# Optimization experiments

Hardware: AMD Instinct MI355X
Metric: run time of the kernel (lower is better)

The kernel has to match this reference:

```python
import jax, jax.numpy as jnp
import numpy as np

B, S, D, H = 2, 2048, 1024, 16
DK = D // H

def setup_inputs() -> dict:
    key = jax.random.key(0)
    ks = jax.random.split(key, 5)
    scale = 1.0 / np.sqrt(D)
    return {
        "query": jax.random.normal(ks[0], (B, S, D), dtype=jnp.float32),
        "mask": jnp.ones((B, S, S), dtype=jnp.int32),
        "Wq": jax.random.normal(ks[1], (D, D), dtype=jnp.float32) * scale,
        "bq": jnp.zeros((D,), dtype=jnp.float32),
        "Wk": jax.random.normal(ks[2], (D, D), dtype=jnp.float32) * scale,
        "bk": jnp.zeros((D,), dtype=jnp.float32),
        "Wv": jax.random.normal(ks[3], (D, D), dtype=jnp.float32) * scale,
        "bv": jnp.zeros((D,), dtype=jnp.float32),
        "Wo": jax.random.normal(ks[4], (D, D), dtype=jnp.float32) * scale,
        "bo": jnp.zeros((D,), dtype=jnp.float32),
    }

def reference(query, mask, Wq, bq, Wk, bk, Wv, bv, Wo, bo):
    # self-attention: key = value = query (torch Linear: x @ W.T + b)
    b, s, d = query.shape
    def proj(x, W, bias):
        y = jnp.einsum('bsd,ed->bse', x, W) + bias
        return y.reshape(b, s, H, DK).transpose(0, 2, 1, 3)  # [B,H,S,DK]
    q = proj(query, Wq, bq)
    k = proj(query, Wk, bk)
    v = proj(query, Wv, bv)
    scores = jnp.einsum('bhqd,bhkd->bhqk', q, k) / jnp.sqrt(jnp.float32(DK))
    m = mask[:, None, :, :]  # [B,1,S,S] (torch unsqueeze(1) for 3D mask)
    scores = jnp.where(m == 0, jnp.float32(-1e9), scores)
    w = jax.nn.softmax(scores, axis=-1)  # dropout: eval mode -> identity
    o = jnp.einsum('bhqk,bhkd->bhqd', w, v)
    o = o.transpose(0, 2, 1, 3).reshape(b, s, d)
    return jnp.einsum('bsd,ed->bse', o, Wo) + bo
```

## Files before the change

### kernel.cpp

```cpp
#include <hip/hip_runtime.h>


typedef _Float16 f16x8 __attribute__((ext_vector_type(8)));
typedef _Float16 f16x4 __attribute__((ext_vector_type(4)));
typedef float    f32x4 __attribute__((ext_vector_type(4)));

#define MFMA16(a, b, c) __builtin_amdgcn_mfma_f32_16x16x32_f16(a, b, c, 0, 0, 0)

__device__ __forceinline__ void gld16(const void* g, void* l) {
    __builtin_amdgcn_global_load_lds(
        (const __attribute__((address_space(1))) void*)g,
        (__attribute__((address_space(3))) void*)l, 16, 0, 0);
}

__global__ void k_conv(const float* __restrict__ in, _Float16* __restrict__ out, int n) {
    int i = (blockIdx.x * 256 + threadIdx.x) * 4;
    if (i >= n) return;
    float4 v = *(const float4*)(in + i);
    f16x4 o;
    o.x = (_Float16)v.x; o.y = (_Float16)v.y; o.z = (_Float16)v.z; o.w = (_Float16)v.w;
    *(f16x4*)(out + i) = o;
}

__global__ void k_maskscan(const int* __restrict__ mask, int* __restrict__ flag) {
    int i = (blockIdx.x * 256 + threadIdx.x) * 4;
    int4 v = *(const int4*)(mask + i);
    if ((v.x == 0) | (v.y == 0) | (v.z == 0) | (v.w == 0)) atomicOr(flag, 1);
}

__global__ __launch_bounds__(256, 2) void k_qkv(
    const _Float16* __restrict__ X,
    const _Float16* __restrict__ Wqh, const _Float16* __restrict__ Wkh,
    const _Float16* __restrict__ Wvh,
    const float* __restrict__ bq, const float* __restrict__ bk,
    const float* __restrict__ bv,
    _Float16* __restrict__ Qo, _Float16* __restrict__ Ko, _Float16* __restrict__ Vo)
{
    __shared__ _Float16 As[128 * 64];
    __shared__ _Float16 Bs[128 * 64];
    const int tid = threadIdx.x;
    const int lane = tid & 63, wv = tid >> 6;
    const int wrow = wv >> 1, wcol = wv & 1;
    const int quad = lane >> 4, lc = lane & 15;
    const int which = blockIdx.x >> 3;
    const _Float16* W   = which == 0 ? Wqh : which == 1 ? Wkh : Wvh;
    const float*   bias = which == 0 ? bq  : which == 1 ? bk  : bv;
    const int n0 = (blockIdx.x & 7) * 128;
    const int m0 = blockIdx.y * 128;

    const f32x4 fzero = {0.f, 0.f, 0.f, 0.f};
    f32x4 acc[4][4];
#pragma unroll
    for (int a = 0; a < 4; ++a)
#pragma unroll
        for (int bb = 0; bb < 4; ++bb) acc[a][bb] = fzero;

#pragma unroll 1
    for (int k0 = 0; k0 < 1024; k0 += 64) {
        __syncthreads();
#pragma unroll
        for (int it = 0; it < 4; ++it) {
            const int wbase = it * 256 + wv * 64;
            const int ci = wbase + lane;
            const int r = ci >> 3;
            const int c8 = (((ci & 7) ^ (r & 7)) * 8);
            gld16(X + (size_t)(m0 + r) * 1024 + k0 + c8, As + wbase * 8);
            gld16(W + (size_t)(n0 + r) * 1024 + k0 + c8, Bs + wbase * 8);
        }
        __syncthreads();
#pragma unroll
        for (int ks = 0; ks < 2; ++ks) {
            f16x8 af[4], bf[4];
#pragma unroll
            for (int mt = 0; mt < 4; ++mt)
                af[mt] = *(const f16x8*)(As + (wrow * 64 + mt * 16 + lc) * 64 +
                                         (((ks * 4 + quad) ^ (lc & 7)) * 8));
#pragma unroll
            for (int nt = 0; nt < 4; ++nt)
                bf[nt] = *(const f16x8*)(Bs + (wcol * 64 + nt * 16 + lc) * 64 +
                                         (((ks * 4 + quad) ^ (lc & 7)) * 8));
#pragma unroll
            for (int mt = 0; mt < 4; ++mt)
#pragma unroll
                for (int nt = 0; nt < 4; ++nt)
                    acc[mt][nt] = MFMA16(af[mt], bf[nt], acc[mt][nt]);
        }
    }
    const float qs = (which == 0) ? 0.18033688011112042f : 1.0f;
    if (which == 2) {
#pragma unroll
        for (int nt = 0; nt < 4; ++nt) {
            const int e = n0 + wcol * 64 + nt * 16 + lc;
            const float bv_ = bias[e];
            const int h = e >> 6, dk = e & 63;
#pragma unroll
            for (int mt = 0; mt < 4; ++mt)
#pragma unroll
                for (int i = 0; i < 4; ++i) {
                    const int m = m0 + wrow * 64 + mt * 16 + quad * 4 + i;
                    const int b_ = m >> 11, s = m & 2047;
                    Vo[(((size_t)b_ * 16 + h) * 64 + dk) * 2048 + s] =
                        (_Float16)(acc[mt][nt][i] + bv_);
                }
        }
    } else {
        _Float16* Out = which == 0 ? Qo : Ko;
#pragma unroll
        for (int nt = 0; nt < 4; ++nt) {
            const int e = n0 + wcol * 64 + nt * 16 + lc;
            const float bv_ = bias[e];
            const int h = e >> 6, dk = e & 63;
#pragma unroll
            for (int mt = 0; mt < 4; ++mt)
#pragma unroll
                for (int i = 0; i < 4; ++i) {
                    const int m = m0 + wrow * 64 + mt * 16 + quad * 4 + i;
                    const int b_ = m >> 11, s = m & 2047;
                    Out[(((size_t)b_ * 16 + h) * 2048 + s) * 64 + dk] =
                        (_Float16)((acc[mt][nt][i] + bv_) * qs);
                }
        }
    }
}

__global__ __launch_bounds__(256, 2) void k_oproj(
    const _Float16* __restrict__ Oin, const _Float16* __restrict__ Woh,
    const float* __restrict__ bo, float* __restrict__ out)
{
    __shared__ _Float16 As[128 * 64];
    __shared__ _Float16 Bs[128 * 64];
    const int tid = threadIdx.x;
    const int lane = tid & 63, wv = tid >> 6;
    const int wrow = wv >> 1, wcol = wv & 1;
    const int quad = lane >> 4, lc = lane & 15;
    const int n0 = blockIdx.x * 128;
    const int m0 = blockIdx.y * 128;

    const f32x4 fzero = {0.f, 0.f, 0.f, 0.f};
    f32x4 acc[4][4];
#pragma unroll
    for (int a = 0; a < 4; ++a)
#pragma unroll
        for (int bb = 0; bb < 4; ++bb) acc[a][bb] = fzero;

#pragma unroll 1
    for (int k0 = 0; k0 < 1024; k0 += 64) {
        __syncthreads();
#pragma unroll
        for (int it = 0; it < 4; ++it) {
            const int wbase = it * 256 + wv * 64;
            const int ci = wbase + lane;
            const int r = ci >> 3;
            const int c8 = (((ci & 7) ^ (r & 7)) * 8);
            gld16(Oin + (size_t)(m0 + r) * 1024 + k0 + c8, As + wbase * 8);
            gld16(Woh + (size_t)(n0 + r) * 1024 + k0 + c8, Bs + wbase * 8);
        }
        __syncthreads();
#pragma unroll
        for (int ks = 0; ks < 2; ++ks) {
            f16x8 af[4], bf[4];
#pragma unroll
            for (int mt = 0; mt < 4; ++mt)
                af[mt] = *(const f16x8*)(As + (wrow * 64 + mt * 16 + lc) * 64 +
                                         (((ks * 4 + quad) ^ (lc & 7)) * 8));
#pragma unroll
            for (int nt = 0; nt < 4; ++nt)
                bf[nt] = *(const f16x8*)(Bs + (wcol * 64 + nt * 16 + lc) * 64 +
                                         (((ks * 4 + quad) ^ (lc & 7)) * 8));
#pragma unroll
            for (int mt = 0; mt < 4; ++mt)
#pragma unroll
                for (int nt = 0; nt < 4; ++nt)
                    acc[mt][nt] = MFMA16(af[mt], bf[nt], acc[mt][nt]);
        }
    }
#pragma unroll
    for (int nt = 0; nt < 4; ++nt) {
        const int e = n0 + wcol * 64 + nt * 16 + lc;
        const float bv_ = bo[e];
#pragma unroll
        for (int mt = 0; mt < 4; ++mt)
#pragma unroll
            for (int i = 0; i < 4; ++i) {
                const int m = m0 + wrow * 64 + mt * 16 + quad * 4 + i;
                out[(size_t)m * 1024 + e] = acc[mt][nt][i] + bv_;
            }
    }
}

__global__ __launch_bounds__(256, 3) void k_attn(
    const _Float16* __restrict__ Q, const _Float16* __restrict__ K,
    const _Float16* __restrict__ Vt, const int* __restrict__ mask,
    const int* __restrict__ flag, _Float16* __restrict__ O)
{
    __shared__ _Float16 Ks[128 * 64];
    __shared__ _Float16 Vs[64 * 128];
    __shared__ _Float16 Ps[4][32 * 64];

    const int tid = threadIdx.x;
    const int lane = tid & 63, wv = tid >> 6;
    const int quad = lane >> 4, lc = lane & 15;
    const int bh = blockIdx.y;
    const int b = bh >> 4, h = bh & 15;
    const int q0 = blockIdx.x * 128;

    const _Float16* Qb = Q  + (size_t)bh * 2048 * 64;
    const _Float16* Kb = K  + (size_t)bh * 2048 * 64;
    const _Float16* Vb = Vt + (size_t)bh * 64 * 2048;

    f16x8 qf[2][2];
#pragma unroll
    for (int nb = 0; nb < 2; ++nb)
#pragma unroll
        for (int ks = 0; ks < 2; ++ks)
            qf[nb][ks] = *(const f16x8*)(Qb + (size_t)(q0 + wv * 32 + nb * 16 + lc) * 64 +
                                         ks * 32 + quad * 8);

    const f32x4 fzero = {0.f, 0.f, 0.f, 0.f};
    f32x4 o[2][4];
    float m_i[2], l_i[2];
#pragma unroll
    for (int nb = 0; nb < 2; ++nb) { m_i[nb] = -1e30f; l_i[nb] = 0.f; }
#pragma unroll
    for (int qb = 0; qb < 2; ++qb)
#pragma unroll
        for (int db = 0; db < 4; ++db) o[qb][db] = fzero;

    const bool has_zero = (*flag != 0);
    _Float16* Pw = Ps[wv];

#pragma unroll 1
    for (int kt = 0; kt < 16; ++kt) {
        const int k0 = kt * 128;
        __syncthreads();
#pragma unroll
        for (int it = 0; it < 4; ++it) {
            const int p = it * 256 + wv * 64 + lane;
            const int r = p >> 3, c = (p & 7) ^ (r & 7);
            gld16(Kb + (size_t)(k0 + r) * 64 + c * 8, Ks + (it * 256 + wv * 64) * 8);
        }
#pragma unroll
        for (int it = 0; it < 4; ++it) {
            const int p = it * 256 + wv * 64 + lane;
            const int dk = p >> 4, c = (p & 15) ^ (dk & 15);
            gld16(Vb + (size_t)dk * 2048 + k0 + c * 8, Vs + (it * 256 + wv * 64) * 8);
        }
        __syncthreads();

        f32x4 st[8][2];
#pragma unroll
        for (int mb = 0; mb < 8; ++mb)
#pragma unroll
            for (int nb = 0; nb < 2; ++nb) st[mb][nb] = fzero;
#pragma unroll
        for (int ks = 0; ks < 2; ++ks)
#pragma unroll
            for (int mb = 0; mb < 8; ++mb) {
                f16x8 kf = *(const f16x8*)(Ks + (mb * 16 + lc) * 64 +
                                           (((ks * 4 + quad) ^ (lc & 7)) * 8));
                st[mb][0] = MFMA16(kf, qf[0][ks], st[mb][0]);
                st[mb][1] = MFMA16(kf, qf[1][ks], st[mb][1]);
            }

        if (has_zero) {
            for (int nb = 0; nb < 2; ++nb) {
                const int q = q0 + wv * 32 + nb * 16 + lc;
                const int* mr = mask + ((size_t)b * 2048 + q) * 2048 + k0;
                for (int mb = 0; mb < 8; ++mb)
                    for (int i = 0; i < 4; ++i)
                        if (mr[mb * 16 + quad * 4 + i] == 0) st[mb][nb][i] = -1e30f;
            }
        }

        float alpha[2];
#pragma unroll
        for (int nb = 0; nb < 2; ++nb) {
            float v = st[0][nb][0];
#pragma unroll
            for (int mb = 0; mb < 8; ++mb)
#pragma unroll
                for (int i = 0; i < 4; ++i) v = fmaxf(v, st[mb][nb][i]);
            v = fmaxf(v, __shfl_xor(v, 16));
            v = fmaxf(v, __shfl_xor(v, 32));
            const float mnew = fmaxf(m_i[nb], v);
            alpha[nb] = exp2f(m_i[nb] - mnew);
            m_i[nb] = mnew;
            float rs = 0.f;
#pragma unroll
            for (int mb = 0; mb < 8; ++mb)
#pragma unroll
                for (int i = 0; i < 4; ++i) {
                    const float p = exp2f(st[mb][nb][i] - mnew);
                    st[mb][nb][i] = p;
                    rs += p;
                }
            rs += __shfl_xor(rs, 16);
            rs += __shfl_xor(rs, 32);
            l_i[nb] = l_i[nb] * alpha[nb] + rs;
        }
#pragma unroll
        for (int qb = 0; qb < 2; ++qb)
#pragma unroll
            for (int i = 0; i < 4; ++i) {
                const float aC = __shfl(alpha[qb], quad * 4 + i);
#pragma unroll
                for (int db = 0; db < 4; ++db) o[qb][db][i] *= aC;
            }

#pragma unroll
        for (int ph = 0; ph < 2; ++ph) {
#pragma unroll
            for (int nb = 0; nb < 2; ++nb) {
                const int r = nb * 16 + lc;
#pragma unroll
                for (int mbl = 0; mbl < 4; ++mbl) {
                    const int mb = ph * 4 + mbl;
                    const int cp = (2 * mbl + (quad >> 1)) ^ (lc & 7);
                    f16x4 pk;
#pragma unroll
                    for (int i = 0; i < 4; ++i) pk[i] = (_Float16)st[mb][nb][i];
                    *(f16x4*)(Pw + r * 64 + cp * 8 + (quad & 1) * 4) = pk;
                }
            }
#pragma unroll
            for (int kcl = 0; kcl < 2; ++kcl) {
                const int kc = ph * 2 + kcl;
                f16x8 pa[2];
#pragma unroll
                for (int qb = 0; qb < 2; ++qb)
                    pa[qb] = *(const f16x8*)(Pw + (qb * 16 + lc) * 64 +
                                             (((kcl * 4 + quad) ^ (lc & 7)) * 8));
#pragma unroll
                for (int db = 0; db < 4; ++db) {
                    f16x8 vf = *(const f16x8*)(Vs + (db * 16 + lc) * 128 +
                                               (((kc * 4 + quad) ^ lc) * 8));
                    o[0][db] = MFMA16(pa[0], vf, o[0][db]);
                    o[1][db] = MFMA16(pa[1], vf, o[1][db]);
                }
            }
        }
    }

#pragma unroll
    for (int qb = 0; qb < 2; ++qb)
#pragma unroll
        for (int i = 0; i < 4; ++i) {
            const float linv = 1.f / __shfl(l_i[qb], quad * 4 + i);
            const int q = q0 + wv * 32 + qb * 16 + quad * 4 + i;
            _Float16* orow = O + ((size_t)b * 2048 + q) * 1024 + h * 64;
#pragma unroll
            for (int db = 0; db < 4; ++db)
                orow[db * 16 + lc] = (_Float16)(o[qb][db][i] * linv);
        }
}

extern "C" void kernel_launch(void* const* d_in, const int* in_sizes, int n_in,
                              void* d_out, int out_size, void* d_ws, size_t ws_size,
                              hipStream_t stream) {
    const float* query = (const float*)d_in[0];
    const int*   mask  = (const int*)d_in[1];
    const float* Wq = (const float*)d_in[2]; const float* bq = (const float*)d_in[3];
    const float* Wk = (const float*)d_in[4]; const float* bk = (const float*)d_in[5];
    const float* Wv = (const float*)d_in[6]; const float* bv = (const float*)d_in[7];
    const float* Wo = (const float*)d_in[8]; const float* bo = (const float*)d_in[9];
    float* out = (float*)d_out;

    char* ws = (char*)d_ws;
    _Float16* Xh  = (_Float16*)(ws);
    _Float16* Wqh = (_Float16*)(ws + 8388608);
    _Float16* Wkh = (_Float16*)(ws + 10485760);
    _Float16* Wvh = (_Float16*)(ws + 12582912);
    _Float16* Woh = (_Float16*)(ws + 14680064);
    _Float16* Qh  = (_Float16*)(ws + 16777216);
    _Float16* Kh  = (_Float16*)(ws + 25165824);
    _Float16* Vh  = (_Float16*)(ws + 33554432);
    _Float16* Oh  = Xh;
    int* flag     = (int*)(ws + 41943040);

    hipMemsetAsync(flag, 0, 4, stream);
    k_maskscan<<<8192, 256, 0, stream>>>(mask, flag);
    k_conv<<<4096, 256, 0, stream>>>(query, Xh, 4194304);
    k_conv<<<1024, 256, 0, stream>>>(Wq, Wqh, 1048576);
    k_conv<<<1024, 256, 0, stream>>>(Wk, Wkh, 1048576);
    k_conv<<<1024, 256, 0, stream>>>(Wv, Wvh, 1048576);
    k_conv<<<1024, 256, 0, stream>>>(Wo, Woh, 1048576);

    k_qkv<<<dim3(24, 32), 256, 0, stream>>>(Xh, Wqh, Wkh, Wvh, bq, bk, bv, Qh, Kh, Vh);
    k_attn<<<dim3(16, 32), 256, 0, stream>>>(Qh, Kh, Vh, mask, flag, Oh);
    k_oproj<<<dim3(8, 32), 256, 0, stream>>>(Oh, Woh, bo, out);
}
```

Baseline: 254.9 us.

## Fuse prep kernels, widen attention blocks to 8 waves, shrink oproj tiles

Merges the mask scan and five fp32-to-fp16 conversion launches into one kernel, which removes launch overhead. The attention kernel now uses 512 threads, each wave owning 16 query rows instead of 32. This lowers register pressure and lets 8 waves share one K/V tile load. The output projection moves to 64x64 tiles with 4x the blocks to fill more CUs, at the cost of less operand reuse. QKV launch bounds are raised to 3 blocks per CU, and the per-wave halving of attention MFMA reuse may offset some of the occupancy gains.

```diff
diff --git a/kernel.cpp b/kernel.cpp
--- a/kernel.cpp
+++ b/kernel.cpp
@@ -13,22 +13,36 @@
         (__attribute__((address_space(3))) void*)l, 16, 0, 0);
 }
 
-__global__ void k_conv(const float* __restrict__ in, _Float16* __restrict__ out, int n) {
-    int i = (blockIdx.x * 256 + threadIdx.x) * 4;
-    if (i >= n) return;
+__device__ __forceinline__ void conv1k(const float* __restrict__ in,
+                                       _Float16* __restrict__ out, int base) {
+    const int i = base + threadIdx.x * 4;
     float4 v = *(const float4*)(in + i);
     f16x4 o;
     o.x = (_Float16)v.x; o.y = (_Float16)v.y; o.z = (_Float16)v.z; o.w = (_Float16)v.w;
     *(f16x4*)(out + i) = o;
 }
 
-__global__ void k_maskscan(const int* __restrict__ mask, int* __restrict__ flag) {
-    int i = (blockIdx.x * 256 + threadIdx.x) * 4;
-    int4 v = *(const int4*)(mask + i);
-    if ((v.x == 0) | (v.y == 0) | (v.z == 0) | (v.w == 0)) atomicOr(flag, 1);
-}
-
-__global__ __launch_bounds__(256, 2) void k_qkv(
+__global__ void k_pre(const float* __restrict__ X, const float* __restrict__ Wq,
+                      const float* __restrict__ Wk, const float* __restrict__ Wv,
+                      const float* __restrict__ Wo,
+                      _Float16* __restrict__ Xh, _Float16* __restrict__ Wqh,
+                      _Float16* __restrict__ Wkh, _Float16* __restrict__ Wvh,
+                      _Float16* __restrict__ Woh,
+                      const int* __restrict__ mask, int* __restrict__ flag) {
+    const int bid = blockIdx.x;
+    if (bid < 4096)      conv1k(X,  Xh,  bid * 1024);
+    else if (bid < 5120) conv1k(Wq, Wqh, (bid - 4096) * 1024);
+    else if (bid < 6144) conv1k(Wk, Wkh, (bid - 5120) * 1024);
+    else if (bid < 7168) conv1k(Wv, Wvh, (bid - 6144) * 1024);
+    else if (bid < 8192) conv1k(Wo, Woh, (bid - 7168) * 1024);
+    else {
+        const int i = (bid - 8192) * 1024 + threadIdx.x * 4;
+        int4 v = *(const int4*)(mask + i);
+        if ((v.x == 0) | (v.y == 0) | (v.z == 0) | (v.w == 0)) atomicOr(flag, 1);
+    }
+}
+
+__global__ __launch_bounds__(256, 3) void k_qkv(
     const _Float16* __restrict__ X,
     const _Float16* __restrict__ Wqh, const _Float16* __restrict__ Wkh,
     const _Float16* __restrict__ Wvh,
@@ -123,79 +137,78 @@
     }
 }
 
-__global__ __launch_bounds__(256, 2) void k_oproj(
+__global__ __launch_bounds__(256, 4) void k_oproj(
     const _Float16* __restrict__ Oin, const _Float16* __restrict__ Woh,
     const float* __restrict__ bo, float* __restrict__ out)
 {
-    __shared__ _Float16 As[128 * 64];
-    __shared__ _Float16 Bs[128 * 64];
+    __shared__ _Float16 As[64 * 64];
+    __shared__ _Float16 Bs[64 * 64];
     const int tid = threadIdx.x;
     const int lane = tid & 63, wv = tid >> 6;
     const int wrow = wv >> 1, wcol = wv & 1;
     const int quad = lane >> 4, lc = lane & 15;
-    const int n0 = blockIdx.x * 128;
-    const int m0 = blockIdx.y * 128;
+    const int n0 = blockIdx.x * 64;
+    const int m0 = blockIdx.y * 64;
 
     const f32x4 fzero = {0.f, 0.f, 0.f, 0.f};
-    f32x4 acc[4][4];
-#pragma unroll
-    for (int a = 0; a < 4; ++a)
-#pragma unroll
-        for (int bb = 0; bb < 4; ++bb) acc[a][bb] = fzero;
+    f32x4 acc[2][2];
+#pragma unroll
+    for (int a = 0; a < 2; ++a)
+#pragma unroll
+        for (int bb = 0; bb < 2; ++bb) acc[a][bb] = fzero;
 
 #pragma unroll 1
     for (int k0 = 0; k0 < 1024; k0 += 64) {
         __syncthreads();
 #pragma unroll
-        for (int it = 0; it < 4; ++it) {
-            const int wbase = it * 256 + wv * 64;
-            const int ci = wbase + lane;
+        for (int it = 0; it < 2; ++it) {
+            const int ci = it * 256 + tid;
             const int r = ci >> 3;
             const int c8 = (((ci & 7) ^ (r & 7)) * 8);
-            gld16(Oin + (size_t)(m0 + r) * 1024 + k0 + c8, As + wbase * 8);
-            gld16(Woh + (size_t)(n0 + r) * 1024 + k0 + c8, Bs + wbase * 8);
+            gld16(Oin + (size_t)(m0 + r) * 1024 + k0 + c8, As + ci * 8);
+            gld16(Woh + (size_t)(n0 + r) * 1024 + k0 + c8, Bs + ci * 8);
         }
         __syncthreads();
 #pragma unroll
         for (int ks = 0; ks < 2; ++ks) {
-            f16x8 af[4], bf[4];
-#pragma unroll
-            for (int mt = 0; mt < 4; ++mt)
-                af[mt] = *(const f16x8*)(As + (wrow * 64 + mt * 16 + lc) * 64 +
+            f16x8 af[2], bf[2];
+#pragma unroll
+            for (int mt = 0; mt < 2; ++mt)
+                af[mt] = *(const f16x8*)(As + (wrow * 32 + mt * 16 + lc) * 64 +
                                          (((ks * 4 + quad) ^ (lc & 7)) * 8));
 #pragma unroll
-            for (int nt = 0; nt < 4; ++nt)
-                bf[nt] = *(const f16x8*)(Bs + (wcol * 64 + nt * 16 + lc) * 64 +
+            for (int nt = 0; nt < 2; ++nt)
+                bf[nt] = *(const f16x8*)(Bs + (wcol * 32 + nt * 16 + lc) * 64 +
                                          (((ks * 4 + quad) ^ (lc & 7)) * 8));
 #pragma unroll
-            for (int mt = 0; mt < 4; ++mt)
-#pragma unroll
-                for (int nt = 0; nt < 4; ++nt)
+            for (int mt = 0; mt < 2; ++mt)
+#pragma unroll
+                for (int nt = 0; nt < 2; ++nt)
                     acc[mt][nt] = MFMA16(af[mt], bf[nt], acc[mt][nt]);
         }
     }
 #pragma unroll
-    for (int nt = 0; nt < 4; ++nt) {
-        const int e = n0 + wcol * 64 + nt * 16 + lc;
+    for (int nt = 0; nt < 2; ++nt) {
+        const int e = n0 + wcol * 32 + nt * 16 + lc;
         const float bv_ = bo[e];
 #pragma unroll
-        for (int mt = 0; mt < 4; ++mt)
-#pragma unroll
-            for (int i = 0; i < 4; ++i) {
-                const int m = m0 + wrow * 64 + mt * 16 + quad * 4 + i;
+        for (int mt = 0; mt < 2; ++mt)
+#pragma unroll
+            for (int i = 0; i < 2 * 2; ++i) {
+                const int m = m0 + wrow * 32 + mt * 16 + quad * 4 + i;
                 out[(size_t)m * 1024 + e] = acc[mt][nt][i] + bv_;
             }
     }
 }
 
-__global__ __launch_bounds__(256, 3) void k_attn(
+__global__ __launch_bounds__(512, 4) void k_attn(
     const _Float16* __restrict__ Q, const _Float16* __restrict__ K,
     const _Float16* __restrict__ Vt, const int* __restrict__ mask,
     const int* __restrict__ flag, _Float16* __restrict__ O)
 {
     __shared__ _Float16 Ks[128 * 64];
     __shared__ _Float16 Vs[64 * 128];
-    __shared__ _Float16 Ps[4][32 * 64];
+    __shared__ _Float16 Ps[8][16 * 64];
 
     const int tid = threadIdx.x;
     const int lane = tid & 63, wv = tid >> 6;
@@ -203,28 +216,22 @@
     const int bh = blockIdx.y;
     const int b = bh >> 4, h = bh & 15;
     const int q0 = blockIdx.x * 128;
+    const int qb = q0 + wv * 16;
 
     const _Float16* Qb = Q  + (size_t)bh * 2048 * 64;
     const _Float16* Kb = K  + (size_t)bh * 2048 * 64;
     const _Float16* Vb = Vt + (size_t)bh * 64 * 2048;
 
-    f16x8 qf[2][2];
-#pragma unroll
-    for (int nb = 0; nb < 2; ++nb)
-#pragma unroll
-        for (int ks = 0; ks < 2; ++ks)
-            qf[nb][ks] = *(const f16x8*)(Qb + (size_t)(q0 + wv * 32 + nb * 16 + lc) * 64 +
-                                         ks * 32 + quad * 8);
+    f16x8 qf[2];
+#pragma unroll
+    for (int ks = 0; ks < 2; ++ks)
+        qf[ks] = *(const f16x8*)(Qb + (size_t)(qb + lc) * 64 + ks * 32 + quad * 8);
 
     const f32x4 fzero = {0.f, 0.f, 0.f, 0.f};
-    f32x4 o[2][4];
-    float m_i[2], l_i[2];
-#pragma unroll
-    for (int nb = 0; nb < 2; ++nb) { m_i[nb] = -1e30f; l_i[nb] = 0.f; }
-#pragma unroll
-    for (int qb = 0; qb < 2; ++qb)
-#pragma unroll
-        for (int db = 0; db < 4; ++db) o[qb][db] = fzero;
+    f32x4 o[4];
+    float m_i = -1e30f, l_i = 0.f;
+#pragma unroll
+    for (int db = 0; db < 4; ++db) o[db] = fzero;
 
     const bool has_zero = (*flag != 0);
     _Float16* Pw = Ps[wv];
@@ -234,124 +241,99 @@
         const int k0 = kt * 128;
         __syncthreads();
 #pragma unroll
-        for (int it = 0; it < 4; ++it) {
-            const int p = it * 256 + wv * 64 + lane;
+        for (int it = 0; it < 2; ++it) {
+            const int p = it * 512 + tid;
             const int r = p >> 3, c = (p & 7) ^ (r & 7);
-            gld16(Kb + (size_t)(k0 + r) * 64 + c * 8, Ks + (it * 256 + wv * 64) * 8);
-        }
-#pragma unroll
-        for (int it = 0; it < 4; ++it) {
-            const int p = it * 256 + wv * 64 + lane;
-            const int dk = p >> 4, c = (p & 15) ^ (dk & 15);
-            gld16(Vb + (size_t)dk * 2048 + k0 + c * 8, Vs + (it * 256 + wv * 64) * 8);
-        }
-        __syncthreads();
-
-        f32x4 st[8][2];
-#pragma unroll
-        for (int mb = 0; mb < 8; ++mb)
-#pragma unroll
-            for (int nb = 0; nb < 2; ++nb) st[mb][nb] = fzero;
+            gld16(Kb + (size_t)(k0 + r) * 64 + c * 8, Ks + p * 8);
+            const int dk = p >> 4, cv = (p & 15) ^ (dk & 15);
+            gld16(Vb + (size_t)dk * 2048 + k0 + cv * 8, Vs + p * 8);
+        }
+        __syncthreads();
+
+        f32x4 st[8];
+#pragma unroll
+        for (int mb = 0; mb < 8; ++mb) st[mb] = fzero;
 #pragma unroll
         for (int ks = 0; ks < 2; ++ks)
 #pragma unroll
             for (int mb = 0; mb < 8; ++mb) {
                 f16x8 kf = *(const f16x8*)(Ks + (mb * 16 + lc) * 64 +
                                            (((ks * 4 + quad) ^ (lc & 7)) * 8));
-                st[mb][0] = MFMA16(kf, qf[0][ks], st[mb][0]);
-                st[mb][1] = MFMA16(kf, qf[1][ks], st[mb][1]);
+                st[mb] = MFMA16(kf, qf[ks], st[mb]);
             }
 
         if (has_zero) {
-            for (int nb = 0; nb < 2; ++nb) {
-                const int q = q0 + wv * 32 + nb * 16 + lc;
-                const int* mr = mask + ((size_t)b * 2048 + q) * 2048 + k0;
-                for (int mb = 0; mb < 8; ++mb)
-                    for (int i = 0; i < 4; ++i)
-                        if (mr[mb * 16 + quad * 4 + i] == 0) st[mb][nb][i] = -1e30f;
-            }
-        }
-
-        float alpha[2];
-#pragma unroll
-        for (int nb = 0; nb < 2; ++nb) {
-            float v = st[0][nb][0];
-#pragma unroll
+            const int q = qb + lc;
+            const int* mr = mask + ((size_t)b * 2048 + q) * 2048 + k0;
             for (int mb = 0; mb < 8; ++mb)
-#pragma unroll
-                for (int i = 0; i < 4; ++i) v = fmaxf(v, st[mb][nb][i]);
-            v = fmaxf(v, __shfl_xor(v, 16));
-            v = fmaxf(v, __shfl_xor(v, 32));
-            const float mnew = fmaxf(m_i[nb], v);
-            alpha[nb] = exp2f(m_i[nb] - mnew);
-            m_i[nb] = mnew;
-            float rs = 0.f;
-#pragma unroll
-            for (int mb = 0; mb < 8; ++mb)
-#pragma unroll
-                for (int i = 0; i < 4; ++i) {
-                    const float p = exp2f(st[mb][nb][i] - mnew);
-                    st[mb][nb][i] = p;
-                    rs += p;
-                }
-            rs += __shfl_xor(rs, 16);
-            rs += __shfl_xor(rs, 32);
-            l_i[nb] = l_i[nb] * alpha[nb] + rs;
-        }
-#pragma unroll
-        for (int qb = 0; qb < 2; ++qb)
+                for (int i = 0; i < 4; ++i)
+                    if (mr[mb * 16 + quad * 4 + i] == 0) st[mb][i] = -1e30f;
+        }
+
+        float v = st[0][0];
+#pragma unroll
+        for (int mb = 0; mb < 8; ++mb)
+#pragma unroll
+            for (int i = 0; i < 4; ++i) v = fmaxf(v, st[mb][i]);
+        v = fmaxf(v, __shfl_xor(v, 16));
+        v = fmaxf(v, __shfl_xor(v, 32));
+        const float mnew = fmaxf(m_i, v);
+        const float alpha = exp2f(m_i - mnew);
+        m_i = mnew;
+        float rs = 0.f;
+#pragma unroll
+        for (int mb = 0; mb < 8; ++mb)
 #pragma unroll
             for (int i = 0; i < 4; ++i) {
-                const float aC = __shfl(alpha[qb], quad * 4 + i);
-#pragma unroll
-                for (int db = 0; db < 4; ++db) o[qb][db][i] *= aC;
-            }
+                const float p = exp2f(st[mb][i] - mnew);
+                st[mb][i] = p;
+                rs += p;
+            }
+        rs += __shfl_xor(rs, 16);
+        rs += __shfl_xor(rs, 32);
+        l_i = l_i * alpha + rs;
+#pragma unroll
+        for (int i = 0; i < 4; ++i) {
+            const float aC = __shfl(alpha, quad * 4 + i);
+#pragma unroll
+            for (int db = 0; db < 4; ++db) o[db][i] *= aC;
+        }
 
 #pragma unroll
         for (int ph = 0; ph < 2; ++ph) {
 #pragma unroll
-            for (int nb = 0; nb < 2; ++nb) {
-                const int r = nb * 16 + lc;
-#pragma unroll
-                for (int mbl = 0; mbl < 4; ++mbl) {
-                    const int mb = ph * 4 + mbl;
-                    const int cp = (2 * mbl + (quad >> 1)) ^ (lc & 7);
-                    f16x4 pk;
-#pragma unroll
-                    for (int i = 0; i < 4; ++i) pk[i] = (_Float16)st[mb][nb][i];
-                    *(f16x4*)(Pw + r * 64 + cp * 8 + (quad & 1) * 4) = pk;
-                }
+            for (int mbl = 0; mbl < 4; ++mbl) {
+                const int mb = ph * 4 + mbl;
+                const int cp = (2 * mbl + (quad >> 1)) ^ (lc & 7);
+                f16x4 pk;
+#pragma unroll
+                for (int i = 0; i < 4; ++i) pk[i] = (_Float16)st[mb][i];
+                *(f16x4*)(Pw + lc * 64 + cp * 8 + (quad & 1) * 4) = pk;
             }
 #pragma unroll
             for (int kcl = 0; kcl < 2; ++kcl) {
                 const int kc = ph * 2 + kcl;
-                f16x8 pa[2];
-#pragma unroll
-                for (int qb = 0; qb < 2; ++qb)
-                    pa[qb] = *(const f16x8*)(Pw + (qb * 16 + lc) * 64 +
-                                             (((kcl * 4 + quad) ^ (lc & 7)) * 8));
+                f16x8 pa = *(const f16x8*)(Pw + lc * 64 +
+                                           (((kcl * 4 + quad) ^ (lc & 7)) * 8));
 #pragma unroll
                 for (int db = 0; db < 4; ++db) {
                     f16x8 vf = *(const f16x8*)(Vs + (db * 16 + lc) * 128 +
                                                (((kc * 4 + quad) ^ lc) * 8));
-                    o[0][db] = MFMA16(pa[0], vf, o[0][db]);
-                    o[1][db] = MFMA16(pa[1], vf, o[1][db]);
+                    o[db] = MFMA16(pa, vf, o[db]);
                 }
             }
         }
     }
 
 #pragma unroll
-    for (int qb = 0; qb < 2; ++qb)
-#pragma unroll
-        for (int i = 0; i < 4; ++i) {
-            const float linv = 1.f / __shfl(l_i[qb], quad * 4 + i);
-            const int q = q0 + wv * 32 + qb * 16 + quad * 4 + i;
-            _Float16* orow = O + ((size_t)b * 2048 + q) * 1024 + h * 64;
-#pragma unroll
-            for (int db = 0; db < 4; ++db)
-                orow[db * 16 + lc] = (_Float16)(o[qb][db][i] * linv);
-        }
+    for (int i = 0; i < 4; ++i) {
+        const float linv = 1.f / __shfl(l_i, quad * 4 + i);
+        const int q = qb + quad * 4 + i;
+        _Float16* orow = O + ((size_t)b * 2048 + q) * 1024 + h * 64;
+#pragma unroll
+        for (int db = 0; db < 4; ++db)
+            orow[db * 16 + lc] = (_Float16)(o[db][i] * linv);
+    }
 }
 
 extern "C" void kernel_launch(void* const* d_in, const int* in_sizes, int n_in,
@@ -378,14 +360,9 @@
     int* flag     = (int*)(ws + 41943040);
 
     hipMemsetAsync(flag, 0, 4, stream);
-    k_maskscan<<<8192, 256, 0, stream>>>(mask, flag);
-    k_conv<<<4096, 256, 0, stream>>>(query, Xh, 4194304);
-    k_conv<<<1024, 256, 0, stream>>>(Wq, Wqh, 1048576);
-    k_conv<<<1024, 256, 0, stream>>>(Wk, Wkh, 1048576);
-    k_conv<<<1024, 256, 0, stream>>>(Wv, Wvh, 1048576);
-    k_conv<<<1024, 256, 0, stream>>>(Wo, Woh, 1048576);
-
+    k_pre<<<16384, 256, 0, stream>>>(query, Wq, Wk, Wv, Wo,
+                                     Xh, Wqh, Wkh, Wvh, Woh, mask, flag);
     k_qkv<<<dim3(24, 32), 256, 0, stream>>>(Xh, Wqh, Wkh, Wvh, bq, bk, bv, Qh, Kh, Vh);
-    k_attn<<<dim3(16, 32), 256, 0, stream>>>(Qh, Kh, Vh, mask, flag, Oh);
-    k_oproj<<<dim3(8, 32), 256, 0, stream>>>(Oh, Woh, bo, out);
-}
+    k_attn<<<dim3(16, 32), 512, 0, stream>>>(Qh, Kh, Vh, mask, flag, Oh);
+    k_oproj<<<dim3(16, 64), 256, 0, stream>>>(Oh, Woh, bo, out);
+}
```

Result: faster. 242.2 us (-5.0%).
